# Optimization experiments

Hardware: AMD Instinct MI355X
Metric: run time of the kernel (lower is better)

## Reference

```python
import jax, jax.numpy as jnp
import numpy as np

B, S, H = 32, 512, 768
N, E, P = 4096, 131072, 65536
HEADS1, C1 = 4, 128
HEADS2, C2 = 1, 64
NUM_REL, REL_HID = 6, 256
NER_HID, NER_LAB = 256, 9
LRELU_SLOPE = 0.2  # PyG GATConv default negative_slope
LN_EPS = 1e-5


def setup_inputs() -> dict:
    key = jax.random.key(0)
    ks = jax.random.split(key, 24)
    sc = 0.02
    inp = {
        'sequence_output': jax.random.normal(ks[0], (B, S, H), jnp.float32),
        'ent_start': jax.random.randint(ks[1], (N,), 0, S - 8),
        'ent_len': jax.random.randint(ks[2], (N,), 0, 8),
        'ent_batch': jax.random.randint(ks[3], (N,), 0, B),
        'edge_index': jax.random.randint(ks[4], (2, E), 0, N),
        'pair_idx': jax.random.randint(ks[5], (P, 2), 0, N),
        'W1': jax.random.normal(ks[6], (H, HEADS1 * C1), jnp.float32) * sc,
        'a_src1': jax.random.normal(ks[7], (HEADS1, C1), jnp.float32) * sc,
        'a_dst1': jax.random.normal(ks[8], (HEADS1, C1), jnp.float32) * sc,
        'b1': jnp.zeros((HEADS1 * C1,), jnp.float32),
        'W2': jax.random.normal(ks[9], (HEADS1 * C1, HEADS2 * C2), jnp.float32) * sc,
        'a_src2': jax.random.normal(ks[10], (HEADS2, C2), jnp.float32) * sc,
        'a_dst2': jax.random.normal(ks[11], (HEADS2, C2), jnp.float32) * sc,
        'b2': jnp.zeros((HEADS2 * C2,), jnp.float32),
        # 6 per-relation classifiers: Linear(128,256)+LN+ReLU+Linear(256,1)
        'relW1': jax.random.normal(ks[12], (NUM_REL, 2 * C2, REL_HID), jnp.float32) * sc,
        'relb1': jnp.zeros((NUM_REL, REL_HID), jnp.float32),
        'ln_g': jnp.ones((NUM_REL, REL_HID), jnp.float32),
        'ln_b': jnp.zeros((NUM_REL, REL_HID), jnp.float32),
        'relW2': jax.random.normal(ks[13], (NUM_REL, REL_HID, 1), jnp.float32) * sc,
        'relb2': jnp.zeros((NUM_REL, 1), jnp.float32),
        # NER head: Linear(768,256)+ReLU+Linear(256,9)
        'nerW1': jax.random.normal(ks[14], (H, NER_HID), jnp.float32) * sc,
        'nerb1': jnp.zeros((NER_HID,), jnp.float32),
        'nerW2': jax.random.normal(ks[15], (NER_HID, NER_LAB), jnp.float32) * sc,
        'nerb2': jnp.zeros((NER_LAB,), jnp.float32),
    }
    return inp


def _gat(x, src, dst, W, a_src, a_dst, b, heads, ch, n):
    # PyG GATConv: per-head linear, additive attention, softmax over incoming edges
    h = (x @ W).reshape(n, heads, ch)                      # [N,Hd,C]
    e_src = jnp.sum(h * a_src, axis=-1)                    # [N,Hd]
    e_dst = jnp.sum(h * a_dst, axis=-1)
    e = jax.nn.leaky_relu(e_src[src] + e_dst[dst], LRELU_SLOPE)  # [E,Hd]
    m = jax.ops.segment_max(e, dst, num_segments=n)
    ex = jnp.exp(e - m[dst])
    denom = jax.ops.segment_sum(ex, dst, num_segments=n)
    alpha = ex / denom[dst]                                # [E,Hd]
    out = jax.ops.segment_sum(alpha[:, :, None] * h[src], dst, num_segments=n)
    return out.reshape(n, heads * ch) + b


def reference(sequence_output, ent_start, ent_len, ent_batch, edge_index, pair_idx,
              W1, a_src1, a_dst1, b1, W2, a_src2, a_dst2, b2,
              relW1, relb1, ln_g, ln_b, relW2, relb2,
              nerW1, nerb1, nerW2, nerb2):
    n = ent_start.shape[0]
    # NER head on the full sequence
    ner_logits = jax.nn.relu(sequence_output @ nerW1 + nerb1) @ nerW2 + nerb2  # [B,S,9]
    # Entity-span mean pooling via exclusive prefix sums (inclusive span start..start+len)
    csum = jnp.cumsum(sequence_output, axis=1)
    csum = jnp.concatenate([jnp.zeros((B, 1, H), sequence_output.dtype), csum], axis=1)  # [B,S+1,H]
    ent_end = ent_start + ent_len
    span_sum = csum[ent_batch, ent_end + 1] - csum[ent_batch, ent_start]  # [N,H]
    x = span_sum / (ent_len + 1).astype(span_sum.dtype)[:, None]
    # add self loops (PyG GATConv default add_self_loops=True)
    loops = jnp.arange(n, dtype=edge_index.dtype)
    src = jnp.concatenate([edge_index[0], loops])
    dst = jnp.concatenate([edge_index[1], loops])
    x = _gat(x, src, dst, W1, a_src1, a_dst1, b1, HEADS1, C1, n)
    x = jax.nn.relu(x)  # dropout p=0.3 is identity in eval mode
    x = _gat(x, src, dst, W2, a_src2, a_dst2, b2, HEADS2, C2, n)  # [N,64]
    # Pair features: cat(x[e1], x[e2]) -> [P,128]
    pair_feat = jnp.concatenate([x[pair_idx[:, 0]], x[pair_idx[:, 1]]], axis=-1)
    # All 6 relation classifiers, vectorized over the relation dim
    hid = jnp.einsum('pf,rfk->rpk', pair_feat, relW1) + relb1[:, None, :]  # [6,P,256]
    mu = jnp.mean(hid, axis=-1, keepdims=True)
    var = jnp.mean(jnp.square(hid - mu), axis=-1, keepdims=True)
    hid = (hid - mu) * jax.lax.rsqrt(var + LN_EPS) * ln_g[:, None, :] + ln_b[:, None, :]
    hid = jax.nn.relu(hid)
    rel_logits = (jnp.einsum('rpk,rko->rpo', hid, relW2) + relb2[:, None, :])[..., 0]  # [6,P]
    return ner_logits, rel_logits
```

## Files before the change

### kernel.cpp

```cpp
#include <hip/hip_runtime.h>
#include <math.h>

#define LRELU 0.2f

constexpr int Bn = 32, Sn = 512, Hn = 768, Nn = 4096, En = 131072, Pn = 65536;
constexpr int ET = En + Nn;

typedef __attribute__((ext_vector_type(8))) short bf16x8;
typedef __attribute__((ext_vector_type(4))) float f32x4;

constexpr size_t OFF_X0  = 0;
constexpr size_t OFF_UV  = 0;
constexpr size_t OFF_H1  = 4194304;
constexpr size_t OFF_X1  = OFF_H1  + 2097152;
constexpr size_t OFF_H2  = OFF_X1  + 2097152;
constexpr size_t OFF_X2  = OFF_H2  + 262144;
constexpr size_t OFF_ES1 = OFF_X2  + 262144;
constexpr size_t OFF_ED1 = OFF_ES1 + 16384;
constexpr size_t OFF_ES2 = OFF_ED1 + 16384;
constexpr size_t OFF_ED2 = OFF_ES2 + 4096;
constexpr size_t OFF_ROW = OFF_ED2 + 4096;
constexpr size_t OFF_CUR = OFF_ROW + 4104;
constexpr size_t OFF_EDG = OFF_CUR + 4096;
constexpr size_t OFF_W1S = OFF_EDG + 135168;
constexpr size_t OFF_NW1S = OFF_W1S + 196608;

__device__ __forceinline__ short f2bf(float f) {
  union { float f; unsigned u; } x; x.f = f;
  unsigned r = x.u + 0x7fff + ((x.u >> 16) & 1);
  return (short)(r >> 16);
}
__device__ __forceinline__ float bf2f(short s) {
  union { unsigned u; float f; } x;
  x.u = ((unsigned)(unsigned short)s) << 16;
  return x.f;
}

__global__ __launch_bounds__(256) void span_pool_k(
    const float* __restrict__ seq, const int* __restrict__ est,
    const int* __restrict__ eln, const int* __restrict__ ebt,
    float* __restrict__ x0) {
  int idx = blockIdx.x * 256 + threadIdx.x;
  if (idx >= Nn * (Hn / 4)) return;
  int e = idx / (Hn / 4);
  int c = (idx % (Hn / 4)) * 4;
  int s0 = est[e], L = eln[e] + 1, b = ebt[e];
  const float* p = seq + ((size_t)b * Sn + s0) * Hn + c;
  float ax = 0, ay = 0, az = 0, aw = 0;
  for (int i = 0; i < L; ++i) {
    float4 v = *(const float4*)(p + (size_t)i * Hn);
    ax += v.x; ay += v.y; az += v.z; aw += v.w;
  }
  float inv = 1.0f / (float)L;
  float4 o; o.x = ax * inv; o.y = ay * inv; o.z = az * inv; o.w = aw * inv;
  *(float4*)&x0[(size_t)e * Hn + c] = o;
}

template <int EPI, int NTW, int KC>
__global__ __launch_bounds__(256) void mfma_gemm_k(
    const float* __restrict__ A, const short* __restrict__ Bswz,
    float* __restrict__ C, const float* __restrict__ bias,
    int M, int K, int N) {
  constexpr int RS = KC + 8;
  __shared__ short at[64 * RS];
  int t = threadIdx.x;
  size_t rowb = (size_t)blockIdx.x * 64;
  int colb = blockIdx.y * (64 * NTW);
  int w = t >> 6, lane = t & 63, quad = lane >> 4, id = lane & 15;
  f32x4 acc[4][NTW];
#pragma unroll
  for (int mt = 0; mt < 4; ++mt)
#pragma unroll
    for (int nt = 0; nt < NTW; ++nt) acc[mt][nt] = (f32x4){0.f, 0.f, 0.f, 0.f};

  for (int k0 = 0; k0 < K; k0 += KC) {
    constexpr int CH = 64 * KC / 8 / 256;
#pragma unroll
    for (int i = 0; i < CH; ++i) {
      int cid = t + i * 256;
      int p = cid / (KC / 8), o8 = (cid % (KC / 8)) * 8;
      const float* src = &A[(rowb + p) * (size_t)K + k0 + o8];
      float4 v0 = *(const float4*)src;
      float4 v1 = *(const float4*)(src + 4);
      bf16x8 bv;
      bv[0] = f2bf(v0.x); bv[1] = f2bf(v0.y); bv[2] = f2bf(v0.z); bv[3] = f2bf(v0.w);
      bv[4] = f2bf(v1.x); bv[5] = f2bf(v1.y); bv[6] = f2bf(v1.z); bv[7] = f2bf(v1.w);
      *(bf16x8*)&at[p * RS + o8] = bv;
    }
    __syncthreads();
#pragma unroll
    for (int kk = 0; kk < KC / 32; ++kk) {
      bf16x8 af[4], bfr[NTW];
#pragma unroll
      for (int mt = 0; mt < 4; ++mt)
        af[mt] = *(const bf16x8*)&at[(mt * 16 + id) * RS + kk * 32 + quad * 8];
#pragma unroll
      for (int nt = 0; nt < NTW; ++nt) {
        int ntg = (colb >> 4) + w * NTW + nt;
        bfr[nt] = *(const bf16x8*)&Bswz[(((size_t)(k0 >> 5) + kk) * (N >> 4) + ntg) * 512 + lane * 8];
      }
#pragma unroll
      for (int mt = 0; mt < 4; ++mt)
#pragma unroll
        for (int nt = 0; nt < NTW; ++nt)
          acc[mt][nt] = __builtin_amdgcn_mfma_f32_16x16x32_bf16(af[mt], bfr[nt], acc[mt][nt], 0, 0, 0);
    }
    __syncthreads();
  }
#pragma unroll
  for (int nt = 0; nt < NTW; ++nt) {
    int col = colb + w * (16 * NTW) + nt * 16 + id;
#pragma unroll
    for (int mt = 0; mt < 4; ++mt) {
#pragma unroll
      for (int reg = 0; reg < 4; ++reg) {
        size_t row = rowb + mt * 16 + quad * 4 + reg;
        float v = acc[mt][nt][reg];
        if (EPI == 2) ((short*)C)[row * (size_t)N + col] = f2bf(v);
        else          C[row * (size_t)N + col] = v;
      }
    }
  }
}

__global__ __launch_bounds__(256) void ner_fused_k(
    const float* __restrict__ A, const short* __restrict__ Bswz,
    const float* __restrict__ W2, const float* __restrict__ b1,
    const float* __restrict__ b2, float* __restrict__ out) {
  constexpr int K = 768;
  constexpr int RS = 136, HS = 264, WS = 260;
  __shared__ short at[64 * RS];
  __shared__ short hid[64 * HS];
  __shared__ float w2t[9 * WS];
  __shared__ float b2l[9];
  int t = threadIdx.x;
  size_t rowb = (size_t)blockIdx.x * 64;
  for (int u = t; u < 2304; u += 256) {
    int k = u / 9, jj = u % 9;
    w2t[jj * WS + k] = W2[u];
  }
  if (t < 9) b2l[t] = b2[t];
  int w = t >> 6, lane = t & 63, quad = lane >> 4, id = lane & 15;
  f32x4 acc[4][4];
#pragma unroll
  for (int mt = 0; mt < 4; ++mt)
#pragma unroll
    for (int nt = 0; nt < 4; ++nt) acc[mt][nt] = (f32x4){0.f, 0.f, 0.f, 0.f};

  for (int k0 = 0; k0 < K; k0 += 128) {
#pragma unroll
    for (int i = 0; i < 4; ++i) {
      int cid = t + i * 256;
      int p = cid >> 4, o8 = (cid & 15) * 8;
      const float* src = &A[(rowb + p) * (size_t)K + k0 + o8];
      float4 v0 = *(const float4*)src;
      float4 v1 = *(const float4*)(src + 4);
      bf16x8 bv;
      bv[0] = f2bf(v0.x); bv[1] = f2bf(v0.y); bv[2] = f2bf(v0.z); bv[3] = f2bf(v0.w);
      bv[4] = f2bf(v1.x); bv[5] = f2bf(v1.y); bv[6] = f2bf(v1.z); bv[7] = f2bf(v1.w);
      *(bf16x8*)&at[p * RS + o8] = bv;
    }
    __syncthreads();
#pragma unroll
    for (int kk = 0; kk < 4; ++kk) {
      bf16x8 af[4], bfr[4];
#pragma unroll
      for (int mt = 0; mt < 4; ++mt)
        af[mt] = *(const bf16x8*)&at[(mt * 16 + id) * RS + kk * 32 + quad * 8];
#pragma unroll
      for (int nt = 0; nt < 4; ++nt) {
        int ntg = w * 4 + nt;
        bfr[nt] = *(const bf16x8*)&Bswz[(((size_t)(k0 >> 5) + kk) * 16 + ntg) * 512 + lane * 8];
      }
#pragma unroll
      for (int mt = 0; mt < 4; ++mt)
#pragma unroll
        for (int nt = 0; nt < 4; ++nt)
          acc[mt][nt] = __builtin_amdgcn_mfma_f32_16x16x32_bf16(af[mt], bfr[nt], acc[mt][nt], 0, 0, 0);
    }
    __syncthreads();
  }
#pragma unroll
  for (int nt = 0; nt < 4; ++nt) {
    int col = w * 64 + nt * 16 + id;
    float bb = b1[col];
#pragma unroll
    for (int mt = 0; mt < 4; ++mt)
#pragma unroll
      for (int reg = 0; reg < 4; ++reg) {
        int row = mt * 16 + quad * 4 + reg;
        hid[row * HS + col] = f2bf(fmaxf(acc[mt][nt][reg] + bb, 0.f));
      }
  }
  __syncthreads();
  for (int u = t; u < 576; u += 256) {
    int row = u / 9, jj = u % 9;
    const short* hp = &hid[row * HS];
    const float* wp = &w2t[jj * WS];
    float a = 0.f;
#pragma unroll
    for (int k8 = 0; k8 < 256; k8 += 8) {
      bf16x8 hv = *(const bf16x8*)&hp[k8];
      float4 w0 = *(const float4*)&wp[k8];
      float4 w1 = *(const float4*)&wp[k8 + 4];
      a += bf2f(hv[0]) * w0.x + bf2f(hv[1]) * w0.y + bf2f(hv[2]) * w0.z + bf2f(hv[3]) * w0.w;
      a += bf2f(hv[4]) * w1.x + bf2f(hv[5]) * w1.y + bf2f(hv[6]) * w1.z + bf2f(hv[7]) * w1.w;
    }
    out[(rowb + row) * 9 + jj] = a + b2l[jj];
  }
}

template <int K, int N>
__global__ void swz_k(const float* __restrict__ B, short* __restrict__ o) {
  int i = blockIdx.x * 256 + threadIdx.x;
  if (i >= K * N) return;
  int n = i % N, k = i / N;
  int kk = k >> 5, quad = (k >> 3) & 3, j = k & 7, ntg = n >> 4, id = n & 15;
  o[(((size_t)kk * (N >> 4)) + ntg) * 512 + (quad * 16 + id) * 8 + j] = f2bf(B[i]);
}

__global__ void swz_uv_k(const float* __restrict__ rW1, short* __restrict__ o) {
  int i = blockIdx.x * 256 + threadIdx.x;
  if (i >= 6 * 128 * 256) return;
  int n = i & 255, k = (i >> 8) & 127, r = i >> 15;
  int c = r * 512 + (k >> 6) * 256 + n;
  int kr = k & 63;
  int kk = kr >> 5, quad = (kr >> 3) & 3, j = kr & 7, ntg = c >> 4, id = c & 15;
  o[(((size_t)kk * 192) + ntg) * 512 + (quad * 16 + id) * 8 + j] = f2bf(rW1[i]);
}

template <int HD, int C>
__global__ __launch_bounds__(256) void coef_b_k(
    const short* __restrict__ h, const float* __restrict__ a_src,
    const float* __restrict__ a_dst, float* __restrict__ es, float* __restrict__ ed) {
  int idx = blockIdx.x * 256 + threadIdx.x;
  if (idx >= Nn * HD) return;
  int n = idx / HD, hd = idx % HD;
  const short* hp = h + (size_t)n * HD * C + hd * C;
  const float* sp = a_src + hd * C;
  const float* dp = a_dst + hd * C;
  float s = 0, d = 0;
  for (int c = 0; c < C; c += 8) {
    bf16x8 v = *(const bf16x8*)(hp + c);
#pragma unroll
    for (int k = 0; k < 8; ++k) {
      float f = bf2f(v[k]);
      s += f * sp[c + k];
      d += f * dp[c + k];
    }
  }
  es[idx] = s; ed[idx] = d;
}

__global__ void zero_k(int* __restrict__ p, int n) {
  int i = blockIdx.x * 256 + threadIdx.x;
  if (i < n) p[i] = 0;
}

__global__ void count_k(const int* __restrict__ eidx, int* __restrict__ cnt) {
  int i = blockIdx.x * 256 + threadIdx.x;
  if (i >= ET) return;
  int dst = (i < En) ? eidx[En + i] : (i - En);
  atomicAdd(&cnt[dst], 1);
}

__global__ __launch_bounds__(256) void scan_k(int* cnt_cur, int* rowoff) {
  __shared__ int s[256];
  int t = threadIdx.x;
  int loc[16]; int run = 0; int base = t * 16;
#pragma unroll
  for (int i = 0; i < 16; ++i) { loc[i] = run; run += cnt_cur[base + i]; }
  s[t] = run;
  __syncthreads();
  for (int off = 1; off < 256; off <<= 1) {
    int v = (t >= off) ? s[t - off] : 0;
    __syncthreads();
    s[t] += v;
    __syncthreads();
  }
  int offset = (t > 0) ? s[t - 1] : 0;
#pragma unroll
  for (int i = 0; i < 16; ++i) {
    int o = offset + loc[i];
    rowoff[base + i] = o;
    cnt_cur[base + i] = o;
  }
  if (t == 255) rowoff[4096] = s[255];
}

__global__ void scatter_k(const int* __restrict__ eidx, int* __restrict__ cur,
                          int* __restrict__ esrc) {
  int i = blockIdx.x * 256 + threadIdx.x;
  if (i >= ET) return;
  int s, d;
  if (i < En) { s = eidx[i]; d = eidx[En + i]; } else { s = d = i - En; }
  int pos = atomicAdd(&cur[d], 1);
  esrc[pos] = s;
}

template <int HD, int C, bool RELU>
__global__ __launch_bounds__(256) void gat_agg_k(
    const short* __restrict__ h, const float* __restrict__ es,
    const float* __restrict__ ed, const int* __restrict__ row_off,
    const int* __restrict__ eslist, const float* __restrict__ bias,
    float* __restrict__ xout) {
  constexpr int HDC = HD * C, OCT = HDC / 8, JS = 256 / OCT;
  constexpr int CAP = 320;
  __shared__ float red[256];
  __shared__ float mxs[HD], dns[HD];
  __shared__ float exc[CAP * HD];
  __shared__ float part[JS * HDC];
  int n = blockIdx.x, t = threadIdx.x;
  int ro = row_off[n], deg = row_off[n + 1] - ro;
  int hd = t % HD, ei = t / HD;
  constexpr int ES = 256 / HD;
  float edv = ed[n * HD + hd];
  float pm = -3.402823466e38f;
  for (int j = ei; j < deg; j += ES) {
    int s = eslist[ro + j];
    float e = es[s * HD + hd] + edv;
    e = (e > 0.f) ? e : LRELU * e;
    pm = fmaxf(pm, e);
  }
  red[t] = pm;
  __syncthreads();
  for (int off = 128; off >= HD; off >>= 1) {
    if (t < off) red[t] = fmaxf(red[t], red[t + off]);
    __syncthreads();
  }
  if (t < HD) mxs[t] = red[t];
  __syncthreads();
  float mx = mxs[hd];
  float ps = 0.f;
  for (int j = ei; j < deg; j += ES) {
    int s = eslist[ro + j];
    float e = es[s * HD + hd] + edv;
    e = (e > 0.f) ? e : LRELU * e;
    float ex = __expf(e - mx);
    if (j < CAP) exc[j * HD + hd] = ex;
    ps += ex;
  }
  red[t] = ps;
  __syncthreads();
  for (int off = 128; off >= HD; off >>= 1) {
    if (t < off) red[t] += red[t + off];
    __syncthreads();
  }
  if (t < HD) dns[t] = red[t];
  __syncthreads();
  int oc = t % OCT, js = t / OCT;
  int hh = oc / (C / 8);
  float mxh = mxs[hh], edh = ed[n * HD + hh];
  float a[8];
#pragma unroll
  for (int k = 0; k < 8; ++k) a[k] = 0.f;
  for (int j = js; j < deg; j += JS) {
    int s = eslist[ro + j];
    float ex;
    if (j < CAP) ex = exc[j * HD + hh];
    else {
      float e = es[s * HD + hh] + edh;
      e = (e > 0.f) ? e : LRELU * e;
      ex = __expf(e - mxh);
    }
    bf16x8 hv = *(const bf16x8*)&h[(size_t)s * HDC + oc * 8];
#pragma unroll
    for (int k = 0; k < 8; ++k) a[k] += ex * bf2f(hv[k]);
  }
#pragma unroll
  for (int k = 0; k < 8; ++k) part[js * HDC + oc * 8 + k] = a[k];
  __syncthreads();
  for (int c = t; c < HDC; c += 256) {
    float sum = 0.f;
#pragma unroll
    for (int q = 0; q < JS; ++q) sum += part[q * HDC + c];
    int hh2 = c / C;
    float v = sum / dns[hh2] + bias[c];
    if (RELU) v = fmaxf(v, 0.f);
    xout[(size_t)n * HDC + c] = v;
  }
}

__global__ __launch_bounds__(256) void pair_rel_k(
    const short* __restrict__ UV, const int* __restrict__ pidx,
    const float* __restrict__ rb1, const float* __restrict__ lng,
    const float* __restrict__ lnb, const float* __restrict__ rW2,
    const float* __restrict__ rb2, float* __restrict__ out) {
  int t = threadIdx.x;
  int r = blockIdx.y;
  int w = t >> 6, lane = t & 63;
  int pg = lane >> 4, l16 = lane & 15;
  float rbl[16], g[16], bb[16], wv[16];
  int cb = r * 256 + l16 * 16;
#pragma unroll
  for (int q = 0; q < 4; ++q) {
    *(float4*)&rbl[q * 4] = *(const float4*)&rb1[cb + q * 4];
    *(float4*)&g[q * 4]   = *(const float4*)&lng[cb + q * 4];
    *(float4*)&bb[q * 4]  = *(const float4*)&lnb[cb + q * 4];
    *(float4*)&wv[q * 4]  = *(const float4*)&rW2[cb + q * 4];
  }
  float rb2v = rb2[r];
  int pbase = blockIdx.x * 256 + w * 64;
  for (int it = 0; it < 16; ++it) {
    int p = pbase + it * 4 + pg;
    int i = pidx[p * 2], j = pidx[p * 2 + 1];
    const short* up = &UV[(size_t)i * 3072 + r * 512 + l16 * 16];
    const short* vp = &UV[(size_t)j * 3072 + r * 512 + 256 + l16 * 16];
    bf16x8 u0 = *(const bf16x8*)up, u1 = *(const bf16x8*)(up + 8);
    bf16x8 v0 = *(const bf16x8*)vp, v1 = *(const bf16x8*)(vp + 8);
    float hv[16], s1 = 0.f, s2 = 0.f;
#pragma unroll
    for (int cc = 0; cc < 8; ++cc) {
      float h = bf2f(u0[cc]) + bf2f(v0[cc]) + rbl[cc];
      hv[cc] = h; s1 += h; s2 += h * h;
    }
#pragma unroll
    for (int cc = 0; cc < 8; ++cc) {
      float h = bf2f(u1[cc]) + bf2f(v1[cc]) + rbl[8 + cc];
      hv[8 + cc] = h; s1 += h; s2 += h * h;
    }
#pragma unroll
    for (int off = 1; off < 16; off <<= 1) {
      s1 += __shfl_xor(s1, off, 64);
      s2 += __shfl_xor(s2, off, 64);
    }
    float mu = s1 * (1.f / 256.f);
    float var = s2 * (1.f / 256.f) - mu * mu;
    float rs = rsqrtf(var + 1e-5f);
    float pv = 0.f;
#pragma unroll
    for (int cc = 0; cc < 16; ++cc) {
      float v = (hv[cc] - mu) * rs * g[cc] + bb[cc];
      v = fmaxf(v, 0.f);
      pv += v * wv[cc];
    }
#pragma unroll
    for (int off = 1; off < 16; off <<= 1) pv += __shfl_xor(pv, off, 64);
    if (l16 == 0) out[(size_t)r * Pn + p] = pv + rb2v;
  }
}

extern "C" void kernel_launch(void* const* d_in, const int* in_sizes, int n_in,
                              void* d_out, int out_size, void* d_ws, size_t ws_size,
                              hipStream_t stream) {
  const float* seq = (const float*)d_in[0];
  const int* est = (const int*)d_in[1];
  const int* eln = (const int*)d_in[2];
  const int* ebt = (const int*)d_in[3];
  const int* eidx = (const int*)d_in[4];
  const int* pidx = (const int*)d_in[5];
  const float* W1 = (const float*)d_in[6];
  const float* as1 = (const float*)d_in[7];
  const float* ad1 = (const float*)d_in[8];
  const float* b1 = (const float*)d_in[9];
  const float* W2 = (const float*)d_in[10];
  const float* as2 = (const float*)d_in[11];
  const float* ad2 = (const float*)d_in[12];
  const float* b2 = (const float*)d_in[13];
  const float* rW1 = (const float*)d_in[14];
  const float* rb1 = (const float*)d_in[15];
  const float* lng = (const float*)d_in[16];
  const float* lnb = (const float*)d_in[17];
  const float* rW2 = (const float*)d_in[18];
  const float* rb2 = (const float*)d_in[19];
  const float* nW1 = (const float*)d_in[20];
  const float* nb1 = (const float*)d_in[21];
  const float* nW2 = (const float*)d_in[22];
  const float* nb2 = (const float*)d_in[23];
  float* out = (float*)d_out;
  float* ws = (float*)d_ws;

  float* x0 = ws + OFF_X0;
  short* uv = (short*)(ws + OFF_UV);
  short* h1 = (short*)(ws + OFF_H1);
  float* x1 = ws + OFF_X1;
  short* h2 = (short*)(ws + OFF_H2);
  short* uvw = (short*)(ws + OFF_H2);
  float* x2 = ws + OFF_X2;
  float* es1 = ws + OFF_ES1;
  float* ed1 = ws + OFF_ED1;
  float* es2 = ws + OFF_ES2;
  float* ed2 = ws + OFF_ED2;
  int* rowoff = (int*)(ws + OFF_ROW);
  int* cur = (int*)(ws + OFF_CUR);
  int* edg = (int*)(ws + OFF_EDG);
  short* w1s = (short*)(ws + OFF_W1S);
  short* w2s = (short*)(ws + OFF_W1S);
  short* nw1s = (short*)(ws + OFF_NW1S);

  zero_k<<<16, 256, 0, stream>>>(cur, Nn);
  count_k<<<(ET + 255) / 256, 256, 0, stream>>>(eidx, cur);
  scan_k<<<1, 256, 0, stream>>>(cur, rowoff);
  scatter_k<<<(ET + 255) / 256, 256, 0, stream>>>(eidx, cur, edg);
  swz_k<768, 512><<<(768 * 512 + 255) / 256, 256, 0, stream>>>(W1, w1s);
  swz_k<768, 256><<<(768 * 256 + 255) / 256, 256, 0, stream>>>(nW1, nw1s);

  span_pool_k<<<Nn * (Hn / 4) / 256, 256, 0, stream>>>(seq, est, eln, ebt, x0);

  mfma_gemm_k<2, 2, 128><<<dim3(Nn / 64, 512 / 128), 256, 0, stream>>>(x0, w1s, (float*)h1, nullptr, Nn, Hn, 512);
  swz_k<512, 64><<<(512 * 64 + 255) / 256, 256, 0, stream>>>(W2, w2s);
  coef_b_k<4, 128><<<(Nn * 4) / 256, 256, 0, stream>>>(h1, as1, ad1, es1, ed1);
  gat_agg_k<4, 128, true><<<Nn, 256, 0, stream>>>(h1, es1, ed1, rowoff, edg, b1, x1);

  mfma_gemm_k<2, 1, 128><<<dim3(Nn / 64, 1), 256, 0, stream>>>(x1, w2s, (float*)h2, nullptr, Nn, 512, 64);
  coef_b_k<1, 64><<<(Nn + 255) / 256, 256, 0, stream>>>(h2, as2, ad2, es2, ed2);
  gat_agg_k<1, 64, false><<<Nn, 256, 0, stream>>>(h2, es2, ed2, rowoff, edg, b2, x2);

  swz_uv_k<<<(6 * 128 * 256) / 256, 256, 0, stream>>>(rW1, uvw);
  mfma_gemm_k<2, 2, 64><<<dim3(Nn / 64, 3072 / 128), 256, 0, stream>>>(x2, uvw, (float*)uv, nullptr, Nn, 64, 3072);
  pair_rel_k<<<dim3(Pn / 256, 6), 256, 0, stream>>>(uv, pidx, rb1, lng, lnb, rW2, rb2,
                                                    out + (size_t)Bn * Sn * 9);

  ner_fused_k<<<(Bn * Sn) / 64, 256, 0, stream>>>(seq, nw1s, nW2, nb1, nb2, out);
}
```

Before: 342.1 us.

## Merge weight swizzles, relayout UV per relation with fused bias, shrink NER tile

Merges the three weight-swizzle kernels into one launch. Changes the UV GEMM epilogue to write a per-relation [r][node][512] layout with the relation bias folded in, so pair_rel reads a smaller contiguous slab per relation and skips the bias add. Templates the fused NER kernel on its row tile and launches it with 32-row tiles, giving more blocks at the cost of reloading the weights more often per row. The aim is to cut launch overhead, improve gather locality and raise occupancy.

```diff
diff --git a/kernel.cpp b/kernel.cpp
--- a/kernel.cpp
+++ b/kernel.cpp
@@ -24,6 +24,7 @@
 constexpr size_t OFF_EDG = OFF_CUR + 4096;
 constexpr size_t OFF_W1S = OFF_EDG + 135168;
 constexpr size_t OFF_NW1S = OFF_W1S + 196608;
+constexpr size_t OFF_W2S = OFF_NW1S + 98304;
 
 __device__ __forceinline__ short f2bf(float f) {
   union { float f; unsigned u; } x; x.f = f;
@@ -116,40 +117,49 @@
       for (int reg = 0; reg < 4; ++reg) {
         size_t row = rowb + mt * 16 + quad * 4 + reg;
         float v = acc[mt][nt][reg];
-        if (EPI == 2) ((short*)C)[row * (size_t)N + col] = f2bf(v);
-        else          C[row * (size_t)N + col] = v;
+        if (EPI == 3) {
+          int r = col >> 9, rem = col & 511;
+          if (rem < 256) v += bias[(r << 8) + rem];
+          ((short*)C)[((size_t)r * Nn + row) * 512 + rem] = f2bf(v);
+        } else if (EPI == 2) {
+          ((short*)C)[row * (size_t)N + col] = f2bf(v);
+        } else {
+          C[row * (size_t)N + col] = v;
+        }
       }
     }
   }
 }
 
+template <int MT>
 __global__ __launch_bounds__(256) void ner_fused_k(
     const float* __restrict__ A, const short* __restrict__ Bswz,
     const float* __restrict__ W2, const float* __restrict__ b1,
     const float* __restrict__ b2, float* __restrict__ out) {
   constexpr int K = 768;
   constexpr int RS = 136, HS = 264, WS = 260;
-  __shared__ short at[64 * RS];
-  __shared__ short hid[64 * HS];
+  constexpr int MW = MT / 16;
+  __shared__ short at[MT * RS];
+  __shared__ short hid[MT * HS];
   __shared__ float w2t[9 * WS];
   __shared__ float b2l[9];
   int t = threadIdx.x;
-  size_t rowb = (size_t)blockIdx.x * 64;
+  size_t rowb = (size_t)blockIdx.x * MT;
   for (int u = t; u < 2304; u += 256) {
     int k = u / 9, jj = u % 9;
     w2t[jj * WS + k] = W2[u];
   }
   if (t < 9) b2l[t] = b2[t];
   int w = t >> 6, lane = t & 63, quad = lane >> 4, id = lane & 15;
-  f32x4 acc[4][4];
-#pragma unroll
-  for (int mt = 0; mt < 4; ++mt)
+  f32x4 acc[MW][4];
+#pragma unroll
+  for (int mt = 0; mt < MW; ++mt)
 #pragma unroll
     for (int nt = 0; nt < 4; ++nt) acc[mt][nt] = (f32x4){0.f, 0.f, 0.f, 0.f};
 
   for (int k0 = 0; k0 < K; k0 += 128) {
 #pragma unroll
-    for (int i = 0; i < 4; ++i) {
+    for (int i = 0; i < MT / 16; ++i) {
       int cid = t + i * 256;
       int p = cid >> 4, o8 = (cid & 15) * 8;
       const float* src = &A[(rowb + p) * (size_t)K + k0 + o8];
@@ -163,9 +173,9 @@
     __syncthreads();
 #pragma unroll
     for (int kk = 0; kk < 4; ++kk) {
-      bf16x8 af[4], bfr[4];
-#pragma unroll
-      for (int mt = 0; mt < 4; ++mt)
+      bf16x8 af[MW], bfr[4];
+#pragma unroll
+      for (int mt = 0; mt < MW; ++mt)
         af[mt] = *(const bf16x8*)&at[(mt * 16 + id) * RS + kk * 32 + quad * 8];
 #pragma unroll
       for (int nt = 0; nt < 4; ++nt) {
@@ -173,7 +183,7 @@
         bfr[nt] = *(const bf16x8*)&Bswz[(((size_t)(k0 >> 5) + kk) * 16 + ntg) * 512 + lane * 8];
       }
 #pragma unroll
-      for (int mt = 0; mt < 4; ++mt)
+      for (int mt = 0; mt < MW; ++mt)
 #pragma unroll
         for (int nt = 0; nt < 4; ++nt)
           acc[mt][nt] = __builtin_amdgcn_mfma_f32_16x16x32_bf16(af[mt], bfr[nt], acc[mt][nt], 0, 0, 0);
@@ -185,7 +195,7 @@
     int col = w * 64 + nt * 16 + id;
     float bb = b1[col];
 #pragma unroll
-    for (int mt = 0; mt < 4; ++mt)
+    for (int mt = 0; mt < MW; ++mt)
 #pragma unroll
       for (int reg = 0; reg < 4; ++reg) {
         int row = mt * 16 + quad * 4 + reg;
@@ -193,7 +203,7 @@
       }
   }
   __syncthreads();
-  for (int u = t; u < 576; u += 256) {
+  for (int u = t; u < MT * 9; u += 256) {
     int row = u / 9, jj = u % 9;
     const short* hp = &hid[row * HS];
     const float* wp = &w2t[jj * WS];
@@ -210,13 +220,24 @@
   }
 }
 
-template <int K, int N>
-__global__ void swz_k(const float* __restrict__ B, short* __restrict__ o) {
+__device__ __forceinline__ void swz_store(short* __restrict__ o, int k, int n, int N, float v) {
+  int kk = k >> 5, quad = (k >> 3) & 3, j = k & 7, ntg = n >> 4, id = n & 15;
+  o[(((size_t)kk * (N >> 4)) + ntg) * 512 + (quad * 16 + id) * 8 + j] = f2bf(v);
+}
+
+__global__ void swz_all_k(const float* __restrict__ W1, const float* __restrict__ nW1,
+                          const float* __restrict__ W2, short* __restrict__ w1s,
+                          short* __restrict__ nw1s, short* __restrict__ w2s) {
   int i = blockIdx.x * 256 + threadIdx.x;
-  if (i >= K * N) return;
-  int n = i % N, k = i / N;
-  int kk = k >> 5, quad = (k >> 3) & 3, j = k & 7, ntg = n >> 4, id = n & 15;
-  o[(((size_t)kk * (N >> 4)) + ntg) * 512 + (quad * 16 + id) * 8 + j] = f2bf(B[i]);
+  if (i < 768 * 512) {
+    swz_store(w1s, i / 512, i % 512, 512, W1[i]);
+  } else if (i < 768 * 512 + 768 * 256) {
+    int i2 = i - 768 * 512;
+    swz_store(nw1s, i2 / 256, i2 % 256, 256, nW1[i2]);
+  } else if (i < 768 * 512 + 768 * 256 + 512 * 64) {
+    int i2 = i - (768 * 512 + 768 * 256);
+    swz_store(w2s, i2 / 64, i2 % 64, 64, W2[i2]);
+  }
 }
 
 __global__ void swz_uv_k(const float* __restrict__ rW1, short* __restrict__ o) {
@@ -383,40 +404,40 @@
 
 __global__ __launch_bounds__(256) void pair_rel_k(
     const short* __restrict__ UV, const int* __restrict__ pidx,
-    const float* __restrict__ rb1, const float* __restrict__ lng,
-    const float* __restrict__ lnb, const float* __restrict__ rW2,
-    const float* __restrict__ rb2, float* __restrict__ out) {
+    const float* __restrict__ lng, const float* __restrict__ lnb,
+    const float* __restrict__ rW2, const float* __restrict__ rb2,
+    float* __restrict__ out) {
   int t = threadIdx.x;
   int r = blockIdx.y;
   int w = t >> 6, lane = t & 63;
   int pg = lane >> 4, l16 = lane & 15;
-  float rbl[16], g[16], bb[16], wv[16];
+  float g[16], bb[16], wv[16];
   int cb = r * 256 + l16 * 16;
 #pragma unroll
   for (int q = 0; q < 4; ++q) {
-    *(float4*)&rbl[q * 4] = *(const float4*)&rb1[cb + q * 4];
-    *(float4*)&g[q * 4]   = *(const float4*)&lng[cb + q * 4];
-    *(float4*)&bb[q * 4]  = *(const float4*)&lnb[cb + q * 4];
-    *(float4*)&wv[q * 4]  = *(const float4*)&rW2[cb + q * 4];
+    *(float4*)&g[q * 4]  = *(const float4*)&lng[cb + q * 4];
+    *(float4*)&bb[q * 4] = *(const float4*)&lnb[cb + q * 4];
+    *(float4*)&wv[q * 4] = *(const float4*)&rW2[cb + q * 4];
   }
   float rb2v = rb2[r];
+  const short* UVr = UV + (size_t)r * Nn * 512;
   int pbase = blockIdx.x * 256 + w * 64;
   for (int it = 0; it < 16; ++it) {
     int p = pbase + it * 4 + pg;
     int i = pidx[p * 2], j = pidx[p * 2 + 1];
-    const short* up = &UV[(size_t)i * 3072 + r * 512 + l16 * 16];
-    const short* vp = &UV[(size_t)j * 3072 + r * 512 + 256 + l16 * 16];
+    const short* up = &UVr[(size_t)i * 512 + l16 * 16];
+    const short* vp = &UVr[(size_t)j * 512 + 256 + l16 * 16];
     bf16x8 u0 = *(const bf16x8*)up, u1 = *(const bf16x8*)(up + 8);
     bf16x8 v0 = *(const bf16x8*)vp, v1 = *(const bf16x8*)(vp + 8);
     float hv[16], s1 = 0.f, s2 = 0.f;
 #pragma unroll
     for (int cc = 0; cc < 8; ++cc) {
-      float h = bf2f(u0[cc]) + bf2f(v0[cc]) + rbl[cc];
+      float h = bf2f(u0[cc]) + bf2f(v0[cc]);
       hv[cc] = h; s1 += h; s2 += h * h;
     }
 #pragma unroll
     for (int cc = 0; cc < 8; ++cc) {
-      float h = bf2f(u1[cc]) + bf2f(v1[cc]) + rbl[8 + cc];
+      float h = bf2f(u1[cc]) + bf2f(v1[cc]);
       hv[8 + cc] = h; s1 += h; s2 += h * h;
     }
 #pragma unroll
@@ -485,20 +506,19 @@
   int* cur = (int*)(ws + OFF_CUR);
   int* edg = (int*)(ws + OFF_EDG);
   short* w1s = (short*)(ws + OFF_W1S);
-  short* w2s = (short*)(ws + OFF_W1S);
   short* nw1s = (short*)(ws + OFF_NW1S);
+  short* w2s = (short*)(ws + OFF_W2S);
 
   zero_k<<<16, 256, 0, stream>>>(cur, Nn);
   count_k<<<(ET + 255) / 256, 256, 0, stream>>>(eidx, cur);
   scan_k<<<1, 256, 0, stream>>>(cur, rowoff);
   scatter_k<<<(ET + 255) / 256, 256, 0, stream>>>(eidx, cur, edg);
-  swz_k<768, 512><<<(768 * 512 + 255) / 256, 256, 0, stream>>>(W1, w1s);
-  swz_k<768, 256><<<(768 * 256 + 255) / 256, 256, 0, stream>>>(nW1, nw1s);
+  swz_all_k<<<(768 * 512 + 768 * 256 + 512 * 64 + 255) / 256, 256, 0, stream>>>(
+      W1, nW1, W2, w1s, nw1s, w2s);
 
   span_pool_k<<<Nn * (Hn / 4) / 256, 256, 0, stream>>>(seq, est, eln, ebt, x0);
 
   mfma_gemm_k<2, 2, 128><<<dim3(Nn / 64, 512 / 128), 256, 0, stream>>>(x0, w1s, (float*)h1, nullptr, Nn, Hn, 512);
-  swz_k<512, 64><<<(512 * 64 + 255) / 256, 256, 0, stream>>>(W2, w2s);
   coef_b_k<4, 128><<<(Nn * 4) / 256, 256, 0, stream>>>(h1, as1, ad1, es1, ed1);
   gat_agg_k<4, 128, true><<<Nn, 256, 0, stream>>>(h1, es1, ed1, rowoff, edg, b1, x1);
 
@@ -507,9 +527,9 @@
   gat_agg_k<1, 64, false><<<Nn, 256, 0, stream>>>(h2, es2, ed2, rowoff, edg, b2, x2);
 
   swz_uv_k<<<(6 * 128 * 256) / 256, 256, 0, stream>>>(rW1, uvw);
-  mfma_gemm_k<2, 2, 64><<<dim3(Nn / 64, 3072 / 128), 256, 0, stream>>>(x2, uvw, (float*)uv, nullptr, Nn, 64, 3072);
-  pair_rel_k<<<dim3(Pn / 256, 6), 256, 0, stream>>>(uv, pidx, rb1, lng, lnb, rW2, rb2,
+  mfma_gemm_k<3, 2, 64><<<dim3(Nn / 64, 3072 / 128), 256, 0, stream>>>(x2, uvw, (float*)uv, rb1, Nn, 64, 3072);
+  pair_rel_k<<<dim3(Pn / 256, 6), 256, 0, stream>>>(uv, pidx, lng, lnb, rW2, rb2,
                                                     out + (size_t)Bn * Sn * 9);
 
-  ner_fused_k<<<(Bn * Sn) / 64, 256, 0, stream>>>(seq, nw1s, nW2, nb1, nb2, out);
-}
+  ner_fused_k<32><<<(Bn * Sn) / 32, 256, 0, stream>>>(seq, nw1s, nW2, nb1, nb2, out);
+}
```

Measured after the change: 347.6 us. About the same (+1.6%).
